# Kernel tuning notes

Hardware: AMD Instinct MI355X
Metric: run time of the kernel (lower is better)

## Reference

```python
import jax, jax.numpy as jnp
import numpy as np

B, N, D = 4, 2048, 1024
H = 16
E = D // H  # 64


def setup_inputs() -> dict:
    key = jax.random.key(0)
    k1, k2, k3 = jax.random.split(key, 3)
    x = jax.random.normal(k1, (B, N, D), dtype=jnp.float32)
    W_qkv = jax.random.normal(k2, (D, 3 * D), dtype=jnp.float32) * 0.02
    W_o = jax.random.normal(k3, (D, D), dtype=jnp.float32) * 0.02
    return {"x": x, "W_qkv": W_qkv, "W_o": W_o}


def reference(x, W_qkv, W_o):
    b, n, d = x.shape
    # QKV projection, then split as 'b n (3 heads e) -> 3 b heads n e'
    qkv = (x @ W_qkv).reshape(b, n, 3, H, E)
    qkv = jnp.transpose(qkv, (2, 0, 3, 1, 4))  # [3, b, H, n, E]
    q, k, v = qkv[0], qkv[1], qkv[2]
    # scores[i, j] = k_i . q_j / sqrt(E)  (note: rows indexed by k-pos, cols by q-pos, as in original)
    scores = jnp.einsum('bhie,bhje->bhij', k, q) / jnp.sqrt(jnp.asarray(E, dtype=x.dtype))
    # original masks strictly-lower-triangular (i > j) entries to -inf
    keep = jnp.triu(jnp.ones((n, n), dtype=bool))  # True where i <= j
    scores = jnp.where(keep, scores, -jnp.inf)
    attn = jax.nn.softmax(scores, axis=-1)  # softmax over last (q/v) axis, as in original
    out = jnp.einsum('bhij,bhje->bhie', attn, v)  # [b, H, n, E]
    out = jnp.transpose(out, (0, 2, 1, 3)).reshape(b, n, H * E)
    return out @ W_o
```

## Files before the change

kernel.cpp:

```cpp
#include <hip/hip_runtime.h>

typedef unsigned short u16;
typedef __bf16 bf16x8 __attribute__((ext_vector_type(8)));
typedef float f32x4 __attribute__((ext_vector_type(4)));
typedef unsigned short u16x4 __attribute__((ext_vector_type(4)));
typedef unsigned short u16x8 __attribute__((ext_vector_type(8)));

__device__ inline u16 f2bf(float f) {
  unsigned u = __builtin_bit_cast(unsigned, f);
  u += 0x7fff + ((u >> 16) & 1);
  return (u16)(u >> 16);
}

__device__ inline f32x4 mfma16(bf16x8 a, bf16x8 b, f32x4 c) {
  return __builtin_amdgcn_mfma_f32_16x16x32_bf16(a, b, c, 0, 0, 0);
}

__device__ inline void async16(const u16* g, u16* l) {
  __builtin_amdgcn_global_load_lds((const __attribute__((address_space(1))) void*)g,
                                   (__attribute__((address_space(3))) void*)l, 16, 0, 0);
}

__global__ __launch_bounds__(256) void k_convert(const float* __restrict__ in,
                                                 u16* __restrict__ out, int n8) {
  int i = blockIdx.x * 256 + threadIdx.x;
  if (i >= n8) return;
  const float4* p = (const float4*)in + 2 * (size_t)i;
  float4 a = p[0], b = p[1];
  u16x8 v;
  v[0] = f2bf(a.x); v[1] = f2bf(a.y); v[2] = f2bf(a.z); v[3] = f2bf(a.w);
  v[4] = f2bf(b.x); v[5] = f2bf(b.y); v[6] = f2bf(b.z); v[7] = f2bf(b.w);
  *((u16x8*)out + i) = v;
}

__global__ __launch_bounds__(256) void k_transpose_conv(const float* __restrict__ in,
                                                        u16* __restrict__ out, int R, int C) {
  __shared__ float t[32][33];
  int c0 = blockIdx.x * 32, r0 = blockIdx.y * 32;
  int lx = threadIdx.x, ly = threadIdx.y;
#pragma unroll
  for (int i = 0; i < 32; i += 8)
    t[ly + i][lx] = in[(size_t)(r0 + ly + i) * C + c0 + lx];
  __syncthreads();
#pragma unroll
  for (int i = 0; i < 32; i += 8)
    out[(size_t)(c0 + ly + i) * R + r0 + lx] = f2bf(t[lx][ly + i]);
}

__global__ __launch_bounds__(256) void k_transpose_v(const u16* __restrict__ V,
                                                     u16* __restrict__ Vt) {
  __shared__ u16 t[64][72];
  int bh = blockIdx.y, n0 = blockIdx.x * 64;
  int tid = threadIdx.x;
  const u16* src = V + (size_t)bh * 2048 * 64;
  u16* dst = Vt + (size_t)bh * 64 * 2048;
#pragma unroll
  for (int half = 0; half < 2; ++half) {
    int f = half * 2048 + tid * 8;
    int r = f >> 6, e = f & 63;
    *(u16x8*)&t[r][e] = *(const u16x8*)&src[(size_t)(n0 + r) * 64 + e];
  }
  __syncthreads();
#pragma unroll
  for (int half = 0; half < 2; ++half) {
    int f = half * 2048 + tid * 8;
    int e = f >> 6, c = f & 63;
    u16x8 v;
#pragma unroll
    for (int j = 0; j < 8; ++j) {
      int tt = c + j;
      v[j] = t[16 * (tt & 3) + (tt >> 2)][e];
    }
    *(u16x8*)&dst[(size_t)e * 2048 + n0 + c] = v;
  }
}

template <int EPI>
__global__ __launch_bounds__(256) void k_gemm(const u16* __restrict__ A,
                                              const u16* __restrict__ Bt,
                                              void* __restrict__ o0, void* __restrict__ o1,
                                              void* __restrict__ o2, int M, int N, int K) {
  __shared__ u16 Al[2][128 * 32];
  __shared__ u16 Bl[2][128 * 32];
  const int tid = threadIdx.x, lane = tid & 63;
  const int row0 = blockIdx.x * 128, col0 = blockIdx.y * 128;
  const int w = tid >> 6;
  const int wr = (w >> 1) * 64, wc = (w & 1) * 64;
  const int l15 = lane & 15, lk = (lane >> 4) * 8;
  const int NK = K >> 5;
  f32x4 acc[4][4] = {};
  const u16* ap0 = A + (size_t)(row0 + (tid >> 2)) * K + (tid & 3) * 8;
  const u16* bp0 = Bt + (size_t)(col0 + (tid >> 2)) * K + (tid & 3) * 8;

#define STAGE(kt, buf)                                       \
  do {                                                       \
    const u16* as = ap0 + (size_t)(kt) * 32;                 \
    const u16* bs = bp0 + (size_t)(kt) * 32;                 \
    async16(as, &Al[buf][tid * 8]);                          \
    async16(as + (size_t)64 * K, &Al[buf][2048 + tid * 8]);  \
    async16(bs, &Bl[buf][tid * 8]);                          \
    async16(bs + (size_t)64 * K, &Bl[buf][2048 + tid * 8]);  \
  } while (0)

  STAGE(0, 0);
  int cur = 0;
  for (int kt = 0; kt < NK; ++kt) {
    __syncthreads();
    if (kt + 1 < NK) STAGE(kt + 1, cur ^ 1);
    bf16x8 af[4], bfr[4];
#pragma unroll
    for (int m = 0; m < 4; ++m)
      af[m] = *(const bf16x8*)&Al[cur][(wr + m * 16 + l15) * 32 + lk];
#pragma unroll
    for (int n = 0; n < 4; ++n)
      bfr[n] = *(const bf16x8*)&Bl[cur][(wc + n * 16 + l15) * 32 + lk];
#pragma unroll
    for (int m = 0; m < 4; ++m)
#pragma unroll
      for (int n = 0; n < 4; ++n) acc[m][n] = mfma16(af[m], bfr[n], acc[m][n]);
    cur ^= 1;
  }
#undef STAGE
#pragma unroll
  for (int m = 0; m < 4; ++m)
#pragma unroll
    for (int n = 0; n < 4; ++n)
#pragma unroll
      for (int r = 0; r < 4; ++r) {
        int gr = row0 + wr + m * 16 + (lane >> 4) * 4 + r;
        int gc = col0 + wc + n * 16 + l15;
        float v = acc[m][n][r];
        if (EPI == 0) {
          int t = gc >> 10, rem = gc & 1023;
          int h = rem >> 6, e = rem & 63;
          int b = gr >> 11, nn = gr & 2047;
          if (t == 1) v *= 0.18033688011112042f;
          u16* dst = (t == 0) ? (u16*)o0 : (t == 1) ? (u16*)o1 : (u16*)o2;
          dst[((size_t)(b * 16 + h) * 2048 + nn) * 64 + e] = f2bf(v);
        } else {
          ((float*)o0)[(size_t)gr * N + gc] = v;
        }
      }
}

__global__ __launch_bounds__(256, 4) void k_attn(const u16* __restrict__ Kg,
                                                 const u16* __restrict__ Qg,
                                                 const u16* __restrict__ Vtg,
                                                 u16* __restrict__ Og) {
  __shared__ u16 Kq[64][72];
  __shared__ u16 Vt[64][72];
  __shared__ u16 Pl[4][32][72];
  const int tid = threadIdx.x, lane = tid & 63, w = tid >> 6;
  const int l15 = lane & 15, lg = lane >> 4;
  const int bx = blockIdx.x, by = blockIdx.y;
  const int r0 = ((bx + 4 * (by >> 4)) & 15) * 128;
  const int bh = by;
  const int wrow = r0 + w * 32;
  const size_t base = (size_t)bh * 2048 * 64;

  bf16x8 qf[2][2];
#pragma unroll
  for (int i0 = 0; i0 < 2; ++i0)
#pragma unroll
    for (int kk = 0; kk < 2; ++kk)
      qf[i0][kk] = *(const bf16x8*)&Kg[base + (size_t)(wrow + i0 * 16 + l15) * 64 + kk * 32 + lg * 8];

  f32x4 acc[2][4] = {};
  float s_part[2][4] = {};

  const int srow = tid >> 2;
  const int scol = (tid & 3) * 16;
  const u16* kp = Qg + base + (size_t)srow * 64 + scol;
  const u16* vp = Vtg + base + (size_t)srow * 2048 + scol;

  u16x8 kr0, kr1, vr0, vr1;
  kr0 = *(const u16x8*)(kp + (size_t)r0 * 64);
  kr1 = *(const u16x8*)(kp + (size_t)r0 * 64 + 8);
  vr0 = *(const u16x8*)(vp + r0);
  vr1 = *(const u16x8*)(vp + r0 + 8);

  for (int j0 = r0; j0 < 2048; j0 += 64) {
    __syncthreads();
    *(u16x8*)&Kq[srow][scol] = kr0;
    *(u16x8*)&Kq[srow][scol + 8] = kr1;
    *(u16x8*)&Vt[srow][scol] = vr0;
    *(u16x8*)&Vt[srow][scol + 8] = vr1;
    __syncthreads();
    int jn = (j0 + 64 < 2048) ? j0 + 64 : j0;
    kr0 = *(const u16x8*)(kp + (size_t)jn * 64);
    kr1 = *(const u16x8*)(kp + (size_t)jn * 64 + 8);
    vr0 = *(const u16x8*)(vp + jn);
    vr1 = *(const u16x8*)(vp + jn + 8);

    if (j0 + 63 < wrow) continue;
    const bool diag = (j0 < wrow + 32);

    f32x4 S[2][4];
#pragma unroll
    for (int jf = 0; jf < 4; ++jf) {
      bf16x8 kf0 = *(const bf16x8*)&Kq[jf * 16 + l15][lg * 8];
      bf16x8 kf1 = *(const bf16x8*)&Kq[jf * 16 + l15][32 + lg * 8];
#pragma unroll
      for (int i0 = 0; i0 < 2; ++i0) {
        f32x4 z = {};
        z = mfma16(qf[i0][0], kf0, z);
        z = mfma16(qf[i0][1], kf1, z);
        S[i0][jf] = z;
      }
    }

#pragma unroll
    for (int i0 = 0; i0 < 2; ++i0)
#pragma unroll
      for (int r = 0; r < 4; ++r) {
        int gi = wrow + i0 * 16 + lg * 4 + r;
        float p0 = __builtin_amdgcn_exp2f(S[i0][0][r]);
        float p1 = __builtin_amdgcn_exp2f(S[i0][1][r]);
        float p2 = __builtin_amdgcn_exp2f(S[i0][2][r]);
        float p3 = __builtin_amdgcn_exp2f(S[i0][3][r]);
        if (diag) {
          p0 = (j0 + l15 >= gi) ? p0 : 0.f;
          p1 = (j0 + 16 + l15 >= gi) ? p1 : 0.f;
          p2 = (j0 + 32 + l15 >= gi) ? p2 : 0.f;
          p3 = (j0 + 48 + l15 >= gi) ? p3 : 0.f;
        }
        s_part[i0][r] += (p0 + p1) + (p2 + p3);
        u16x4 pk;
        pk[0] = f2bf(p0); pk[1] = f2bf(p1); pk[2] = f2bf(p2); pk[3] = f2bf(p3);
        *(u16x4*)&Pl[w][i0 * 16 + lg * 4 + r][4 * l15] = pk;
      }

    bf16x8 pa[2][2];
#pragma unroll
    for (int i0 = 0; i0 < 2; ++i0) {
      pa[i0][0] = *(const bf16x8*)&Pl[w][i0 * 16 + l15][lg * 8];
      pa[i0][1] = *(const bf16x8*)&Pl[w][i0 * 16 + l15][32 + lg * 8];
    }
#pragma unroll
    for (int ef = 0; ef < 4; ++ef) {
      bf16x8 vb0 = *(const bf16x8*)&Vt[ef * 16 + l15][lg * 8];
      bf16x8 vb1 = *(const bf16x8*)&Vt[ef * 16 + l15][32 + lg * 8];
#pragma unroll
      for (int i0 = 0; i0 < 2; ++i0) {
        acc[i0][ef] = mfma16(pa[i0][0], vb0, acc[i0][ef]);
        acc[i0][ef] = mfma16(pa[i0][1], vb1, acc[i0][ef]);
      }
    }
  }

#pragma unroll
  for (int i0 = 0; i0 < 2; ++i0)
#pragma unroll
    for (int r = 0; r < 4; ++r) {
      float s = s_part[i0][r];
#pragma unroll
      for (int d = 1; d < 16; d <<= 1) s += __shfl_xor(s, d);
      s_part[i0][r] = 1.0f / s;
    }
  const size_t obase = ((size_t)(bh >> 4) * 2048) * 1024 + (size_t)(bh & 15) * 64;
#pragma unroll
  for (int i0 = 0; i0 < 2; ++i0)
#pragma unroll
    for (int ef = 0; ef < 4; ++ef)
#pragma unroll
      for (int r = 0; r < 4; ++r) {
        int gi = wrow + i0 * 16 + lg * 4 + r;
        Og[obase + (size_t)gi * 1024 + ef * 16 + l15] = f2bf(acc[i0][ef][r] * s_part[i0][r]);
      }
}

extern "C" void kernel_launch(void* const* d_in, const int* in_sizes, int n_in,
                              void* d_out, int out_size, void* d_ws, size_t ws_size,
                              hipStream_t stream) {
  const float* x = (const float*)d_in[0];
  const float* Wqkv = (const float*)d_in[1];
  const float* Wo = (const float*)d_in[2];
  char* ws = (char*)d_ws;
  u16* x_bf = (u16*)(ws);
  u16* Wq_t = (u16*)(ws + 16777216);
  u16* Wo_t = (u16*)(ws + 23068672);
  u16* Q = (u16*)(ws + 25165824);
  u16* Kx = (u16*)(ws + 41943040);
  u16* V = (u16*)(ws + 58720256);
  u16* Vt = (u16*)(ws + 75497472);
  u16* O = (u16*)(ws + 92274688);

  k_convert<<<8192 * 1024 / 8 / 256, 256, 0, stream>>>(x, x_bf, 8192 * 1024 / 8);
  k_transpose_conv<<<dim3(3072 / 32, 1024 / 32), dim3(32, 8), 0, stream>>>(Wqkv, Wq_t, 1024, 3072);
  k_transpose_conv<<<dim3(1024 / 32, 1024 / 32), dim3(32, 8), 0, stream>>>(Wo, Wo_t, 1024, 1024);
  k_gemm<0><<<dim3(64, 24), 256, 0, stream>>>(x_bf, Wq_t, Q, Kx, V, 8192, 3072, 1024);
  k_transpose_v<<<dim3(32, 64), 256, 0, stream>>>(V, Vt);
  k_attn<<<dim3(16, 64), 256, 0, stream>>>(Kx, Q, Vt, O);
  k_gemm<1><<<dim3(64, 8), 256, 0, stream>>>(O, Wo_t, d_out, nullptr, nullptr, 8192, 1024, 1024);
}
```

Baseline: 290.2 us.

## Keep attention probabilities in registers via transposed MFMA and permuted V layout

The attention kernel now computes S transposed (K-tile as A operand) so each lane holds the right elements to pack P directly into bf16 MFMA operands with perm instructions. This removes the per-wave LDS round trip for P. To match, the V transpose kernel writes V columns in a permuted order so the P·V MFMA lines up with the register layout. The row-sum reduction shrinks to two shuffles, and the output is staged through LDS so global stores are 16-byte vectorized. It also drops the occupancy hint from launch bounds and truncates rather than rounds P to bf16.

Measured after the change: 270.0 us. -7.0%, faster.

```diff
diff --git a/kernel.cpp b/kernel.cpp
--- a/kernel.cpp
+++ b/kernel.cpp
@@ -1,15 +1,22 @@
 #include <hip/hip_runtime.h>
 
 typedef unsigned short u16;
+typedef unsigned int u32;
 typedef __bf16 bf16x8 __attribute__((ext_vector_type(8)));
 typedef float f32x4 __attribute__((ext_vector_type(4)));
 typedef unsigned short u16x4 __attribute__((ext_vector_type(4)));
 typedef unsigned short u16x8 __attribute__((ext_vector_type(8)));
+typedef u32 u32x4 __attribute__((ext_vector_type(4)));
 
 __device__ inline u16 f2bf(float f) {
   unsigned u = __builtin_bit_cast(unsigned, f);
   u += 0x7fff + ((u >> 16) & 1);
   return (u16)(u >> 16);
+}
+
+__device__ inline u32 pk2(float e1, float e0) {
+  return __builtin_amdgcn_perm(__builtin_bit_cast(u32, e1), __builtin_bit_cast(u32, e0),
+                               0x07060302u);
 }
 
 __device__ inline f32x4 mfma16(bf16x8 a, bf16x8 b, f32x4 c) {
@@ -35,7 +42,7 @@
 
 __global__ __launch_bounds__(256) void k_transpose_conv(const float* __restrict__ in,
                                                         u16* __restrict__ out, int R, int C) {
-  __shared__ float t[32][33];
+  __shared__ __align__(16) float t[32][33];
   int c0 = blockIdx.x * 32, r0 = blockIdx.y * 32;
   int lx = threadIdx.x, ly = threadIdx.y;
 #pragma unroll
@@ -49,7 +56,7 @@
 
 __global__ __launch_bounds__(256) void k_transpose_v(const u16* __restrict__ V,
                                                      u16* __restrict__ Vt) {
-  __shared__ u16 t[64][72];
+  __shared__ __align__(16) u16 t[64][72];
   int bh = blockIdx.y, n0 = blockIdx.x * 64;
   int tid = threadIdx.x;
   const u16* src = V + (size_t)bh * 2048 * 64;
@@ -69,7 +76,8 @@
 #pragma unroll
     for (int j = 0; j < 8; ++j) {
       int tt = c + j;
-      v[j] = t[16 * (tt & 3) + (tt >> 2)][e];
+      int tk = tt >> 5, lgk = (tt >> 3) & 3, rem = tt & 7;
+      v[j] = t[16 * (2 * (rem >> 2) + tk) + 4 * lgk + (rem & 3)][e];
     }
     *(u16x8*)&dst[(size_t)e * 2048 + n0 + c] = v;
   }
@@ -80,8 +88,8 @@
                                               const u16* __restrict__ Bt,
                                               void* __restrict__ o0, void* __restrict__ o1,
                                               void* __restrict__ o2, int M, int N, int K) {
-  __shared__ u16 Al[2][128 * 32];
-  __shared__ u16 Bl[2][128 * 32];
+  __shared__ __align__(16) u16 Al[2][128 * 32];
+  __shared__ __align__(16) u16 Bl[2][128 * 32];
   const int tid = threadIdx.x, lane = tid & 63;
   const int row0 = blockIdx.x * 128, col0 = blockIdx.y * 128;
   const int w = tid >> 6;
@@ -143,13 +151,13 @@
       }
 }
 
-__global__ __launch_bounds__(256, 4) void k_attn(const u16* __restrict__ Kg,
-                                                 const u16* __restrict__ Qg,
-                                                 const u16* __restrict__ Vtg,
-                                                 u16* __restrict__ Og) {
-  __shared__ u16 Kq[64][72];
-  __shared__ u16 Vt[64][72];
-  __shared__ u16 Pl[4][32][72];
+__global__ __launch_bounds__(256) void k_attn(const u16* __restrict__ Kg,
+                                              const u16* __restrict__ Qg,
+                                              const u16* __restrict__ Vtg,
+                                              u16* __restrict__ Og) {
+  __shared__ __align__(16) u16 Kq[64][72];
+  __shared__ __align__(16) u16 Vt[64][72];
+  __shared__ __align__(16) u16 Ost[4][32][72];
   const int tid = threadIdx.x, lane = tid & 63, w = tid >> 6;
   const int l15 = lane & 15, lg = lane >> 4;
   const int bx = blockIdx.x, by = blockIdx.y;
@@ -166,7 +174,7 @@
       qf[i0][kk] = *(const bf16x8*)&Kg[base + (size_t)(wrow + i0 * 16 + l15) * 64 + kk * 32 + lg * 8];
 
   f32x4 acc[2][4] = {};
-  float s_part[2][4] = {};
+  f32x4 s4[2] = {};
 
   const int srow = tid >> 2;
   const int scol = (tid & 3) * 16;
@@ -195,78 +203,83 @@
     if (j0 + 63 < wrow) continue;
     const bool diag = (j0 < wrow + 32);
 
-    f32x4 S[2][4];
+    f32x4 Px[2][4];
 #pragma unroll
     for (int jf = 0; jf < 4; ++jf) {
-      bf16x8 kf0 = *(const bf16x8*)&Kq[jf * 16 + l15][lg * 8];
-      bf16x8 kf1 = *(const bf16x8*)&Kq[jf * 16 + l15][32 + lg * 8];
+      bf16x8 a0 = *(const bf16x8*)&Kq[jf * 16 + l15][lg * 8];
+      bf16x8 a1 = *(const bf16x8*)&Kq[jf * 16 + l15][32 + lg * 8];
 #pragma unroll
       for (int i0 = 0; i0 < 2; ++i0) {
         f32x4 z = {};
-        z = mfma16(qf[i0][0], kf0, z);
-        z = mfma16(qf[i0][1], kf1, z);
-        S[i0][jf] = z;
+        z = mfma16(a0, qf[i0][0], z);
+        z = mfma16(a1, qf[i0][1], z);
+        f32x4 e;
+#pragma unroll
+        for (int r = 0; r < 4; ++r) e[r] = __builtin_amdgcn_exp2f(z[r]);
+        if (diag) {
+          int jb = j0 + jf * 16 + lg * 4;
+          int ib = wrow + i0 * 16 + l15;
+#pragma unroll
+          for (int r = 0; r < 4; ++r) e[r] = (jb + r >= ib) ? e[r] : 0.f;
+        }
+        Px[i0][jf] = e;
       }
     }
-
 #pragma unroll
     for (int i0 = 0; i0 < 2; ++i0)
-#pragma unroll
-      for (int r = 0; r < 4; ++r) {
-        int gi = wrow + i0 * 16 + lg * 4 + r;
-        float p0 = __builtin_amdgcn_exp2f(S[i0][0][r]);
-        float p1 = __builtin_amdgcn_exp2f(S[i0][1][r]);
-        float p2 = __builtin_amdgcn_exp2f(S[i0][2][r]);
-        float p3 = __builtin_amdgcn_exp2f(S[i0][3][r]);
-        if (diag) {
-          p0 = (j0 + l15 >= gi) ? p0 : 0.f;
-          p1 = (j0 + 16 + l15 >= gi) ? p1 : 0.f;
-          p2 = (j0 + 32 + l15 >= gi) ? p2 : 0.f;
-          p3 = (j0 + 48 + l15 >= gi) ? p3 : 0.f;
-        }
-        s_part[i0][r] += (p0 + p1) + (p2 + p3);
-        u16x4 pk;
-        pk[0] = f2bf(p0); pk[1] = f2bf(p1); pk[2] = f2bf(p2); pk[3] = f2bf(p3);
-        *(u16x4*)&Pl[w][i0 * 16 + lg * 4 + r][4 * l15] = pk;
+      s4[i0] += (Px[i0][0] + Px[i0][1]) + (Px[i0][2] + Px[i0][3]);
+
+    bf16x8 pb[2][2];
+#pragma unroll
+    for (int i0 = 0; i0 < 2; ++i0)
+#pragma unroll
+      for (int t = 0; t < 2; ++t) {
+        u32x4 wv;
+        wv[0] = pk2(Px[i0][t][1], Px[i0][t][0]);
+        wv[1] = pk2(Px[i0][t][3], Px[i0][t][2]);
+        wv[2] = pk2(Px[i0][t + 2][1], Px[i0][t + 2][0]);
+        wv[3] = pk2(Px[i0][t + 2][3], Px[i0][t + 2][2]);
+        pb[i0][t] = __builtin_bit_cast(bf16x8, wv);
       }
 
-    bf16x8 pa[2][2];
-#pragma unroll
-    for (int i0 = 0; i0 < 2; ++i0) {
-      pa[i0][0] = *(const bf16x8*)&Pl[w][i0 * 16 + l15][lg * 8];
-      pa[i0][1] = *(const bf16x8*)&Pl[w][i0 * 16 + l15][32 + lg * 8];
-    }
 #pragma unroll
     for (int ef = 0; ef < 4; ++ef) {
-      bf16x8 vb0 = *(const bf16x8*)&Vt[ef * 16 + l15][lg * 8];
-      bf16x8 vb1 = *(const bf16x8*)&Vt[ef * 16 + l15][32 + lg * 8];
+      bf16x8 v0 = *(const bf16x8*)&Vt[ef * 16 + l15][lg * 8];
+      bf16x8 v1 = *(const bf16x8*)&Vt[ef * 16 + l15][32 + lg * 8];
 #pragma unroll
       for (int i0 = 0; i0 < 2; ++i0) {
-        acc[i0][ef] = mfma16(pa[i0][0], vb0, acc[i0][ef]);
-        acc[i0][ef] = mfma16(pa[i0][1], vb1, acc[i0][ef]);
+        acc[i0][ef] = mfma16(v0, pb[i0][0], acc[i0][ef]);
+        acc[i0][ef] = mfma16(v1, pb[i0][1], acc[i0][ef]);
       }
     }
   }
 
+  float sc[2];
+#pragma unroll
+  for (int i0 = 0; i0 < 2; ++i0) {
+    f32x4 s = s4[i0];
+    float ss = (s[0] + s[1]) + (s[2] + s[3]);
+    ss += __shfl_xor(ss, 16);
+    ss += __shfl_xor(ss, 32);
+    sc[i0] = 1.0f / ss;
+  }
+
+  u16* ep = &Ost[w][0][0];
 #pragma unroll
   for (int i0 = 0; i0 < 2; ++i0)
 #pragma unroll
-    for (int r = 0; r < 4; ++r) {
-      float s = s_part[i0][r];
-#pragma unroll
-      for (int d = 1; d < 16; d <<= 1) s += __shfl_xor(s, d);
-      s_part[i0][r] = 1.0f / s;
+    for (int ef = 0; ef < 4; ++ef) {
+      u16x4 pk;
+#pragma unroll
+      for (int r = 0; r < 4; ++r) pk[r] = f2bf(acc[i0][ef][r] * sc[i0]);
+      *(u16x4*)&ep[(i0 * 16 + l15) * 72 + ef * 16 + lg * 4] = pk;
     }
-  const size_t obase = ((size_t)(bh >> 4) * 2048) * 1024 + (size_t)(bh & 15) * 64;
-#pragma unroll
-  for (int i0 = 0; i0 < 2; ++i0)
-#pragma unroll
-    for (int ef = 0; ef < 4; ++ef)
-#pragma unroll
-      for (int r = 0; r < 4; ++r) {
-        int gi = wrow + i0 * 16 + lg * 4 + r;
-        Og[obase + (size_t)gi * 1024 + ef * 16 + l15] = f2bf(acc[i0][ef][r] * s_part[i0][r]);
-      }
+  const int orow = lane >> 1, ohalf = lane & 1;
+  const int gi = wrow + orow;
+  u16* od = Og + (size_t)(bh >> 4) * 2048 * 1024 + (size_t)gi * 1024 + (bh & 15) * 64 + ohalf * 32;
+#pragma unroll
+  for (int s = 0; s < 4; ++s)
+    *(u16x8*)&od[s * 8] = *(const u16x8*)&ep[orow * 72 + ohalf * 32 + s * 8];
 }
 
 extern "C" void kernel_launch(void* const* d_in, const int* in_sizes, int n_in,
```
